# Performance work log

Measured on AMD Instinct MI355X. Metric: run time of the kernel, lower is better.

The kernel has to match this reference:

```python
import jax, jax.numpy as jnp
import numpy as np

V, E, D, L, B, EX = 50000, 128, 256, 400, 64, 200


def setup_inputs() -> dict:
    key = jax.random.key(0)
    ks = jax.random.split(key, 32)
    u = lambda k, shp, s=0.02: jax.random.uniform(k, shp, jnp.float32, -s, s)
    inp = {
        'input': jax.random.randint(ks[0], (B, 1), 0, V),
        'hidden_h': jax.random.normal(ks[1], (2, B, D), jnp.float32),
        'hidden_c': jax.random.normal(ks[2], (2, B, D), jnp.float32),
        'encoder_output': jax.random.normal(ks[3], (B, L, 2 * D), jnp.float32),
        'previous_context': jax.random.normal(ks[4], (B, 1, 2 * D), jnp.float32),
        'extended_input': jax.random.randint(ks[5], (B, L), 0, V + EX),
        'coverage': jax.random.uniform(ks[6], (B, L), jnp.float32),
        'padding_mask': jnp.ones((B, L), jnp.float32),
        'ex_size': EX,
        'output_step': 0,
        # parameters
        'emb_w': jax.random.normal(ks[7], (V, E), jnp.float32) * 1e-4,
        'lin_w': u(ks[8], (D, E + 2 * D)), 'lin_b': jnp.zeros((D,), jnp.float32),
        'w_ih': u(ks[9], (4 * D, D)), 'w_hh': u(ks[10], (4 * D, D)),
        'b_ih': jnp.zeros((4 * D,), jnp.float32).at[D:2 * D].set(1.0),
        'b_hh': jnp.zeros((4 * D,), jnp.float32),
        'red_h_w': u(ks[11], (D, 2 * D)), 'red_h_b': jnp.zeros((D,), jnp.float32),
        'red_c_w': u(ks[12], (D, 2 * D)), 'red_c_b': jnp.zeros((D,), jnp.float32),
        'wq_w': u(ks[13], (D, 2 * D)), 'wq_b': jnp.zeros((D,), jnp.float32),
        'cov_w': u(ks[14], (2 * D, 1)), 'cov_b': jnp.zeros((2 * D,), jnp.float32),
        'wk_w': u(ks[15], (D, 2 * D)), 'wk_b': jnp.zeros((D,), jnp.float32),
        'pre_w': u(ks[16], (D, 3 * D)), 'pre_b': jnp.zeros((D,), jnp.float32),
        'gen_w': u(ks[17], (V, D)), 'gen_b': jnp.zeros((V,), jnp.float32),
        'pgen_w': u(ks[18], (1, 5 * D)), 'pgen_b': jnp.zeros((1,), jnp.float32),
    }
    return inp


def reference(input, hidden_h, hidden_c, encoder_output, previous_context,
              extended_input, coverage, padding_mask, ex_size, output_step,
              emb_w, lin_w, lin_b, w_ih, w_hh, b_ih, b_hh,
              red_h_w, red_h_b, red_c_w, red_c_b,
              wq_w, wq_b, cov_w, cov_b, wk_w, wk_b,
              pre_w, pre_b, gen_w, gen_b, pgen_w, pgen_b):
    b = encoder_output.shape[0]
    d = w_ih.shape[1]
    scale = jnp.sqrt(jnp.float32(d))

    emb = emb_w[input[:, 0]][:, None, :]                      # [B,1,E]
    combine = jnp.concatenate([emb, previous_context], 2)     # [B,1,E+2D]
    x = combine @ lin_w.T + lin_b                             # [B,1,D]

    if output_step == 0:  # reduce bidirectional encoder state [2,B,D] -> [1,B,D]
        hs = jnp.transpose(hidden_h, (1, 0, 2)).reshape(b, 2 * d)
        cs = jnp.transpose(hidden_c, (1, 0, 2)).reshape(b, 2 * d)
        h = jax.nn.relu(hs @ red_h_w.T + red_h_b)
        c = jax.nn.relu(cs @ red_c_w.T + red_c_b)
    else:
        h, c = hidden_h[0], hidden_c[0]

    # single LSTM step (PyTorch gate order i,f,g,o)
    gates = x[:, 0] @ w_ih.T + b_ih + h @ w_hh.T + b_hh       # [B,4D]
    i, f, g, o = jnp.split(gates, 4, axis=1)
    c_new = jax.nn.sigmoid(f) * c + jax.nn.sigmoid(i) * jnp.tanh(g)
    h_new = jax.nn.sigmoid(o) * jnp.tanh(c_new)
    lstm_out = h_new[:, None, :]                              # [B,1,D]

    # scaled-dot coverage attention
    query = jnp.concatenate([h_new, c_new], 1)                # [B,2D]
    Q = jnp.tanh(query @ wq_w.T + wq_b)                       # [B,D]
    word_feature = encoder_output + (coverage[..., None] @ cov_w.T + cov_b)
    K = jnp.tanh(word_feature @ wk_w.T + wk_b)                # [B,L,D]
    score = jnp.einsum('bd,bld->bl', Q / scale, K)
    score = jnp.where(padding_mask > 0, score, jnp.float32(-1e18))
    attention = jax.nn.softmax(score, axis=1)                 # [B,L]
    weighted_context = jnp.einsum('bl,bld->bd', attention, encoder_output)[:, None, :]

    p_gen = jax.nn.sigmoid(
        jnp.concatenate([x[:, 0], weighted_context[:, 0], h_new, c_new], 1)
        @ pgen_w.T + pgen_b)                                  # [B,1]

    owc = jnp.concatenate([weighted_context, lstm_out], 2)[:, 0]  # [B,3D]
    pregen = owc @ pre_w.T + pre_b                            # [B,D]
    vocab_dist = p_gen * jax.nn.softmax(pregen @ gen_w.T + gen_b, axis=1)
    att_dist = (1.0 - p_gen) * attention                      # [B,L]

    vocab_ext = jnp.concatenate(
        [vocab_dist, jnp.zeros((b, ex_size), vocab_dist.dtype)], 1)
    final_dist = vocab_ext.at[jnp.arange(b)[:, None], extended_input].add(att_dist)

    hidden = (h_new[None], c_new[None])
    return (final_dist, hidden, weighted_context, attention, coverage, p_gen)
```

## Files before the change

kernel.cpp:

```cpp
#include <hip/hip_runtime.h>
#include <math.h>

#define BB 64
#define DD 256
#define LL 400
#define VV 50000
#define EE 128
#define NB 782

typedef __attribute__((ext_vector_type(8))) short short8v;
typedef __attribute__((ext_vector_type(4))) short short4v;
typedef __attribute__((ext_vector_type(4))) float f32x4;

__device__ __forceinline__ float sigmoidf_(float x){ return 1.0f/(1.0f+expf(-x)); }

__device__ __forceinline__ short f2bf(float f){
    unsigned u = __builtin_bit_cast(unsigned, f);
    u += 0x7fffu + ((u>>16)&1u);
    return (short)(u>>16);
}
__device__ __forceinline__ float bf2f(unsigned short b){
    unsigned u = ((unsigned)b) << 16;
    return __builtin_bit_cast(float, u);
}

#define ROW_X   0
#define ROW_WC  256
#define ROW_H   768
#define ROW_C   1024

#define DOT8(col, wptr, kk, acc) { \
    float a0_=(col)[((kk)+0)*64], a1_=(col)[((kk)+1)*64], a2_=(col)[((kk)+2)*64], a3_=(col)[((kk)+3)*64], \
          a4_=(col)[((kk)+4)*64], a5_=(col)[((kk)+5)*64], a6_=(col)[((kk)+6)*64], a7_=(col)[((kk)+7)*64]; \
    asm volatile("" : "+v"(a0_),"+v"(a1_),"+v"(a2_),"+v"(a3_),"+v"(a4_),"+v"(a5_),"+v"(a6_),"+v"(a7_)); \
    acc += a0_*(wptr)[(kk)+0] + a1_*(wptr)[(kk)+1] + a2_*(wptr)[(kk)+2] + a3_*(wptr)[(kk)+3] \
         + a4_*(wptr)[(kk)+4] + a5_*(wptr)[(kk)+5] + a6_*(wptr)[(kk)+6] + a7_*(wptr)[(kk)+7]; }

__device__ __forceinline__ float dot4v(f32x4 a, f32x4 b){
    return a[0]*b[0] + a[1]*b[1] + a[2]*b[2] + a[3]*b[3];
}

__global__ __launch_bounds__(256) void k_front1(
    const int* __restrict__ inp, const float* __restrict__ hh, const float* __restrict__ hc,
    const float* __restrict__ prev, const float* __restrict__ emb_w,
    const float* __restrict__ lin_w, const float* __restrict__ lin_b,
    const float* __restrict__ rhw, const float* __restrict__ rhb,
    const float* __restrict__ rcw, const float* __restrict__ rcb,
    const int* __restrict__ step_p,
    const float* __restrict__ wk_w, const float* __restrict__ wk_b,
    const float* __restrict__ cov_w, const float* __restrict__ cov_b,
    float* __restrict__ actT, float* __restrict__ WhT, float* __restrict__ WcT0,
    short* __restrict__ Wb, float* __restrict__ u, float* __restrict__ v2,
    float* __restrict__ wcpart, float* __restrict__ Ssum)
{
    const int d = blockIdx.x, y = blockIdx.y, t = threadIdx.x;
    const int b = t >> 2, kq = t & 3;
    __shared__ float lw[640];
    __shared__ float red[256];

    if (y == 3){
        if (t < 128) wcpart[d*128 + t] = 0.f;
        if (d == 0 && t >= 128 && t < 192) Ssum[t-128] = 0.f;
        const float* row = wk_w + (size_t)d*512;
        float su=0.f, sv=0.f;
        for (int j=t; j<512; j+=256){
            float wv = row[j];
            Wb[(size_t)(j>>3)*2048 + d*8 + (j&7)] = f2bf(wv);
            su += wv*cov_w[j];
            sv += wv*cov_b[j];
        }
        float* rs = lw;
        float* rv = red;
        rs[t]=su; rv[t]=sv; __syncthreads();
        for (int s=128;s>0;s>>=1){ if(t<s){rs[t]+=rs[t+s]; rv[t]+=rv[t+s];} __syncthreads(); }
        if (t==0){ u[d]=rs[0]; v2[d]=rv[0] + wk_b[d]; }
        return;
    }

    if (y == 0){
        if (t < 160) ((f32x4*)lw)[t] = ((const f32x4*)(lin_w + (size_t)d*640))[t];
        __syncthreads();
        const f32x4* lw4 = (const f32x4*)lw;
        const f32x4* er4 = (const f32x4*)(emb_w + (size_t)inp[b]*EE);
        const f32x4* pv4 = (const f32x4*)(prev + (size_t)b*512);
        float acc = 0.f;
        for (int i=kq; i<160; i+=16){
            f32x4 v0 = (i    < 32) ? er4[i]    : pv4[i-32];
            f32x4 v1 = (i+4  < 32) ? er4[i+4]  : pv4[i-28];
            f32x4 v2_ = pv4[i-24];
            f32x4 v3 = pv4[i-20];
            if (i+8  < 32) v2_ = er4[i+8];
            if (i+12 < 32) v3 = er4[i+12];
            asm volatile("" : "+v"(v0),"+v"(v1),"+v"(v2_),"+v"(v3));
            acc += dot4v(v0, lw4[i]) + dot4v(v1, lw4[i+4])
                 + dot4v(v2_, lw4[i+8]) + dot4v(v3, lw4[i+12]);
        }
        acc += __shfl_xor(acc,1); acc += __shfl_xor(acc,2);
        if (kq == 0) actT[(ROW_X + d)*64 + b] = lin_b[d] + acc;
        return;
    }

    const float* src  = (y==1) ? hh  : hc;
    float*       dstT = (y==1) ? WhT : WcT0;
    if (*step_p == 0){
        const float* wrow = ((y==1) ? rhw : rcw) + (size_t)d*512;
        const float  bias = ((y==1) ? rhb : rcb)[d];
        if (t < 128) ((f32x4*)lw)[t] = ((const f32x4*)wrow)[t];
        __syncthreads();
        const f32x4* lw4 = (const f32x4*)lw;
        const f32x4* s0 = (const f32x4*)(src + (size_t)b*DD);
        const f32x4* s1 = (const f32x4*)(src + (size_t)BB*DD + (size_t)b*DD);
        float acc = 0.f;
        for (int i=kq; i<128; i+=16){
            f32x4 v0 = (i    < 64) ? s0[i]    : s1[i-64];
            f32x4 v1 = (i+4  < 64) ? s0[i+4]  : s1[i-60];
            f32x4 v2_ = (i+8 < 64) ? s0[i+8]  : s1[i-56];
            f32x4 v3 = (i+12 < 64) ? s0[i+12] : s1[i-52];
            asm volatile("" : "+v"(v0),"+v"(v1),"+v"(v2_),"+v"(v3));
            acc += dot4v(v0, lw4[i]) + dot4v(v1, lw4[i+4])
                 + dot4v(v2_, lw4[i+8]) + dot4v(v3, lw4[i+12]);
        }
        acc += __shfl_xor(acc,1); acc += __shfl_xor(acc,2);
        if (kq == 0){
            float a = bias + acc;
            dstT[d*64 + b] = a>0.f ? a : 0.f;
        }
    } else {
        if (t < 64) dstT[d*64 + t] = src[(size_t)t*DD + d];
    }
}

__global__ __launch_bounds__(256) void k_gl(
    const float* __restrict__ actT, const float* __restrict__ WhT, const float* __restrict__ WcT0,
    const float* __restrict__ w_ih, const float* __restrict__ w_hh,
    const float* __restrict__ b_ih, const float* __restrict__ b_hh,
    float* __restrict__ o_h, float* __restrict__ o_c, float* __restrict__ actT_out)
{
    const int d = blockIdx.x, t = threadIdx.x;
    const int b = t & 63, gi = t >> 6;
    __shared__ float wih[4][256];
    __shared__ float whh[4][256];
    __shared__ float gl[4][64];

    const int gr = gi*DD + d;
    ((f32x4*)&wih[gi][0])[b] = ((const f32x4*)(w_ih + (size_t)gr*DD))[b];
    ((f32x4*)&whh[gi][0])[b] = ((const f32x4*)(w_hh + (size_t)gr*DD))[b];
    __syncthreads();

    const float* xcol = actT + ROW_X*64 + b;
    const float* hcol = WhT + b;
    float a0=0.f, a1=0.f;
    for (int kk=0; kk<256; kk+=8){
        DOT8(xcol, &wih[gi][0], kk, a0);
        DOT8(hcol, &whh[gi][0], kk, a1);
    }
    gl[gi][b] = a0 + a1 + b_ih[gr] + b_hh[gr];
    __syncthreads();

    if (t < 64){
        float iv = sigmoidf_(gl[0][t]);
        float fv = sigmoidf_(gl[1][t]);
        float gv = tanhf(gl[2][t]);
        float ov = sigmoidf_(gl[3][t]);
        float cn = fv*WcT0[d*64 + t] + iv*gv;
        float hn = ov*tanhf(cn);
        o_c[(size_t)t*DD + d] = cn;
        o_h[(size_t)t*DD + d] = hn;
        actT_out[(ROW_C + d)*64 + t] = cn;
        actT_out[(ROW_H + d)*64 + t] = hn;
    }
}

__global__ __launch_bounds__(256) void k_q2(
    const float* __restrict__ actT,
    const float* __restrict__ wq_w, const float* __restrict__ wq_b,
    float* __restrict__ Qs)
{
    const int d = blockIdx.x, t = threadIdx.x;
    const int b = t & 63, w = t >> 6;
    __shared__ float lw[512];
    __shared__ float red[4][64];
    if (t < 128) ((f32x4*)lw)[t] = ((const f32x4*)(wq_w + (size_t)d*512))[t];
    __syncthreads();
    const float* col = actT + ROW_H*64 + b;
    float acc = 0.f;
    const int k0 = w*128;
    for (int kk=k0; kk<k0+128; kk+=8)
        DOT8(col, lw, kk, acc);
    red[w][b] = acc; __syncthreads();
    if (t < 64)
        Qs[(size_t)t*DD + d] = tanhf(wq_b[d] + red[0][t]+red[1][t]+red[2][t]+red[3][t]) * 0.0625f;
}

#define SC_MFMA(KS, BF) \
  { const int cc_ = (KS)*4 + qw; \
    short8v a0_ = *(const short8v*)&As[lr*512 + ((cc_ ^ (lr&7))<<3)]; \
    short8v a1_ = *(const short8v*)&As[(16+lr)*512 + ((cc_ ^ (lr&7))<<3)]; \
    acc0 = __builtin_amdgcn_mfma_f32_16x16x32_bf16(a0_, BF, acc0, 0,0,0); \
    acc1 = __builtin_amdgcn_mfma_f32_16x16x32_bf16(a1_, BF, acc1, 0,0,0); }

#define SC_CHUNK(KC, B0,B1,B2,B3) \
    SC_MFMA((KC)*4+0, B0); SC_MFMA((KC)*4+1, B1); \
    SC_MFMA((KC)*4+2, B2); SC_MFMA((KC)*4+3, B3);

__global__ __launch_bounds__(1024, 4) void k_score_mfma(
    const float* __restrict__ enc, const short* __restrict__ Wb,
    const float* __restrict__ u, const float* __restrict__ v2,
    const float* __restrict__ Qs, const float* __restrict__ cov,
    const float* __restrict__ pmask,
    float* __restrict__ Ev, float* __restrict__ Ssum, float* __restrict__ wcpart)
{
    const int b  = blockIdx.y;
    const int l0 = blockIdx.x * 32;
    const int tid = threadIdx.x;
    const int wave = tid >> 6, lane = tid & 63;
    const int qw = lane >> 4, lr = lane & 15;
    const int col = wave*16 + lr;

    __shared__ __align__(16) short As[32*512];
    __shared__ float Red[16][32];
    __shared__ float esh[32];

    const short* bp = Wb + (size_t)qw*2048 + col*8;
    short8v c0 = *(const short8v*)(bp +  0*8192);
    short8v c1 = *(const short8v*)(bp +  1*8192);
    short8v c2 = *(const short8v*)(bp +  2*8192);
    short8v c3 = *(const short8v*)(bp +  3*8192);

    const int arow = tid >> 5;
    const int af   = tid & 31;
    const bool aval = (l0 + arow) < LL;
    const float4* aptr = (const float4*)(enc + ((size_t)(b*LL + (aval ? l0+arow : 0)))*512);
    float4 areg[4];
    #pragma unroll
    for (int j=0; j<4; j++)
        areg[j] = aval ? aptr[af + j*32] : float4{0.f,0.f,0.f,0.f};

    #pragma unroll
    for (int j=0; j<4; j++){
        const int fi   = af + j*32;
        const int c    = fi >> 1;
        const int half = fi & 1;
        const int cs   = c ^ (arow & 7);
        short4v t4;
        t4[0]=f2bf(areg[j].x); t4[1]=f2bf(areg[j].y);
        t4[2]=f2bf(areg[j].z); t4[3]=f2bf(areg[j].w);
        *(short4v*)&As[arow*512 + cs*8 + half*4] = t4;
    }
    __syncthreads();

    f32x4 acc0 = f32x4{0.f,0.f,0.f,0.f};
    f32x4 acc1 = f32x4{0.f,0.f,0.f,0.f};

    short8v n0 = *(const short8v*)(bp +  4*8192);
    short8v n1 = *(const short8v*)(bp +  5*8192);
    short8v n2 = *(const short8v*)(bp +  6*8192);
    short8v n3 = *(const short8v*)(bp +  7*8192);
    SC_CHUNK(0, c0,c1,c2,c3);
    asm volatile("" : "+v"(n0),"+v"(n1),"+v"(n2),"+v"(n3));

    c0 = *(const short8v*)(bp +  8*8192);
    c1 = *(const short8v*)(bp +  9*8192);
    c2 = *(const short8v*)(bp + 10*8192);
    c3 = *(const short8v*)(bp + 11*8192);
    SC_CHUNK(1, n0,n1,n2,n3);
    asm volatile("" : "+v"(c0),"+v"(c1),"+v"(c2),"+v"(c3));

    n0 = *(const short8v*)(bp + 12*8192);
    n1 = *(const short8v*)(bp + 13*8192);
    n2 = *(const short8v*)(bp + 14*8192);
    n3 = *(const short8v*)(bp + 15*8192);
    SC_CHUNK(2, c0,c1,c2,c3);
    asm volatile("" : "+v"(n0),"+v"(n1),"+v"(n2),"+v"(n3));

    SC_CHUNK(3, n0,n1,n2,n3);

    const float qv = Qs[b*DD + col];
    const float uv = u[col];
    const float vv = v2[col];
    #pragma unroll
    for (int rf=0; rf<2; rf++){
        const f32x4 acc = rf ? acc1 : acc0;
        const int rbase = l0 + rf*16 + qw*4;
        float cv[4];
        if (rbase < LL){
            float4 c4v = *(const float4*)(cov + (size_t)b*LL + rbase);
            cv[0]=c4v.x; cv[1]=c4v.y; cv[2]=c4v.z; cv[3]=c4v.w;
        } else { cv[0]=cv[1]=cv[2]=cv[3]=0.f; }
        #pragma unroll
        for (int r=0; r<4; r++){
            float s = qv * tanhf(acc[r] + cv[r]*uv + vv);
            s += __shfl_xor(s,1); s += __shfl_xor(s,2);
            s += __shfl_xor(s,4); s += __shfl_xor(s,8);
            if (lr == 0) Red[wave][rf*16 + qw*4 + r] = s;
        }
    }
    __syncthreads();
    if (tid < 32){
        int l = l0 + tid;
        float e = 0.f;
        if (l < LL){
            float s = 0.f;
            #pragma unroll
            for (int w2=0; w2<16; w2++) s += Red[w2][tid];
            e = (pmask[b*LL+l] > 0.f) ? expf(s) : 0.f;
            Ev[b*LL + l] = e;
        }
        esh[tid] = e;
        float se = e;
        se += __shfl_xor(se,1); se += __shfl_xor(se,2);
        se += __shfl_xor(se,4); se += __shfl_xor(se,8);
        se += __shfl_xor(se,16);
        if (tid == 0) atomicAdd(&Ssum[b], se);
    }
    __syncthreads();
    if (tid < 512){
        const int c  = tid >> 3;
        const int p  = tid & 7;
        float acc = 0.f;
        #pragma unroll
        for (int l=0; l<32; l++){
            unsigned short bits = (unsigned short)As[l*512 + ((c ^ (l&7))<<3) + p];
            acc += esh[l] * bf2f(bits);
        }
        atomicAdd(&wcpart[b*512 + tid], acc);
    }
}

__global__ __launch_bounds__(512) void k_attn(
    const float* __restrict__ Ev, const float* __restrict__ Ssum,
    const float* __restrict__ cov_in,
    float* __restrict__ attn_out, float* __restrict__ cov_out)
{
    const int b = blockIdx.x, t = threadIdx.x;
    if (t < LL){
        const float inv = 1.0f / Ssum[b];
        attn_out[b*LL + t] = Ev[b*LL + t] * inv;
        cov_out[b*LL + t]  = cov_in[b*LL + t];
    }
}

__global__ __launch_bounds__(256) void k_tr(const float* __restrict__ wcpart,
                                            const float* __restrict__ Ssum,
                                            float* __restrict__ o_wc,
                                            float* __restrict__ actT)
{
    const int j0 = blockIdx.x * 64;
    __shared__ float tile[64][65];
    __shared__ float invs[64];
    const int t = threadIdx.x;
    const int c = t & 63, r0 = t >> 6;
    if (t < 64) invs[t] = 1.0f / Ssum[t];
    __syncthreads();
    #pragma unroll
    for (int bb = r0; bb < 64; bb += 4){
        float v = wcpart[(size_t)bb*512 + j0 + c] * invs[bb];
        tile[bb][c] = v;
        o_wc[(size_t)bb*512 + j0 + c] = v;
    }
    __syncthreads();
    #pragma unroll
    for (int jj = r0; jj < 64; jj += 4)
        actT[(ROW_WC + j0 + jj)*64 + c] = tile[c][jj];
}

__global__ __launch_bounds__(256) void k_pregen(
    const float* __restrict__ actT,
    const float* __restrict__ pre_w, const float* __restrict__ pre_b,
    const float* __restrict__ pgen_w, const float* __restrict__ pgen_b,
    short* __restrict__ pregenb, float* __restrict__ pgen_out)
{
    const int d = blockIdx.x, t = threadIdx.x;
    const int b = t & 63, w = t >> 6;
    __shared__ float pw[768];
    __shared__ float red[4][64];
    if (t < 192) ((f32x4*)pw)[t] = ((const f32x4*)(pre_w + (size_t)d*768))[t];
    __syncthreads();
    const float* col = actT + ROW_WC*64 + b;
    float acc = 0.f;
    const int k0 = w*192;
    for (int kk=k0; kk<k0+192; kk+=8)
        DOT8(col, pw, kk, acc);
    red[w][b] = acc; __syncthreads();
    if (t < 64)
        pregenb[(size_t)t*DD + d] = f2bf(pre_b[d] + red[0][t]+red[1][t]+red[2][t]+red[3][t]);

    if (blockIdx.x == 0){
        __syncthreads();
        const float* colx = actT + b;
        float p = 0.f;
        const int j0 = w*320;
        for (int jj=j0; jj<j0+320; jj+=8)
            DOT8(colx, pgen_w, jj, p);
        red[w][b] = p; __syncthreads();
        if (t < 64)
            pgen_out[t] = sigmoidf_(red[0][t]+red[1][t]+red[2][t]+red[3][t] + pgen_b[0]);
    }
}

#define GEN_SLICE(KS, RA, RB) \
  { short8v bb_; \
    bb_[0]=f2bf(RA[0]); bb_[1]=f2bf(RA[1]); bb_[2]=f2bf(RA[2]); bb_[3]=f2bf(RA[3]); \
    bb_[4]=f2bf(RB[0]); bb_[5]=f2bf(RB[1]); bb_[6]=f2bf(RB[2]); bb_[7]=f2bf(RB[3]); \
    const int cc_ = (KS)*4 + qw; \
    const int cs_ = (cc_ ^ (lr&7))<<3; \
    short8v aa0_ = *(const short8v*)&As[(lr     )*256 + cs_]; \
    short8v aa1_ = *(const short8v*)&As[(16+lr)*256 + cs_]; \
    short8v aa2_ = *(const short8v*)&As[(32+lr)*256 + cs_]; \
    short8v aa3_ = *(const short8v*)&As[(48+lr)*256 + cs_]; \
    acc0 = __builtin_amdgcn_mfma_f32_16x16x32_bf16(aa0_, bb_, acc0, 0,0,0); \
    acc1 = __builtin_amdgcn_mfma_f32_16x16x32_bf16(aa1_, bb_, acc1, 0,0,0); \
    acc2 = __builtin_amdgcn_mfma_f32_16x16x32_bf16(aa2_, bb_, acc2, 0,0,0); \
    acc3 = __builtin_amdgcn_mfma_f32_16x16x32_bf16(aa3_, bb_, acc3, 0,0,0); }

__global__ __launch_bounds__(256, 3) void k_gen_mfma(
    const short* __restrict__ pregenb, const float* __restrict__ gen_w,
    const float* __restrict__ gen_b, short* __restrict__ lgb,
    float* __restrict__ blkM, float* __restrict__ blkS)
{
    const int blk = blockIdx.x;
    const int v0 = blk * 64;
    const int tid = threadIdx.x;
    const int wave = tid>>6, lane = tid&63, qw = lane>>4, lr = lane&15;

    __shared__ __align__(16) short As[64*256];
    __shared__ float pm[4][64];
    __shared__ float ps[4][64];

    const int vrow = v0 + wave*16 + lr;
    const bool bval = (vrow < VV);
    const f32x4* bq = (const f32x4*)(gen_w + (size_t)(bval ? vrow : 0)*DD + qw*8);
    f32x4 a0 = bq[ 0], a1 = bq[ 1];
    f32x4 a2 = bq[ 8], a3 = bq[ 9];
    f32x4 a4 = bq[16], a5 = bq[17];
    f32x4 a6 = bq[24], a7 = bq[25];

    #pragma unroll
    for (int j=0; j<8; j++){
        int f = tid + j*256;
        int row = f >> 5, c = f & 31;
        short8v s = ((const short8v*)pregenb)[f];
        *(short8v*)&As[row*256 + ((c ^ (row&7))<<3)] = s;
    }
    __syncthreads();

    f32x4 acc0 = f32x4{0.f,0.f,0.f,0.f};
    f32x4 acc1 = f32x4{0.f,0.f,0.f,0.f};
    f32x4 acc2 = f32x4{0.f,0.f,0.f,0.f};
    f32x4 acc3 = f32x4{0.f,0.f,0.f,0.f};

    f32x4 b0 = bq[32], b1 = bq[33];
    f32x4 b2 = bq[40], b3 = bq[41];
    f32x4 b4 = bq[48], b5 = bq[49];
    f32x4 b6 = bq[56], b7 = bq[57];

    GEN_SLICE(0, a0, a1);
    GEN_SLICE(1, a2, a3);
    GEN_SLICE(2, a4, a5);
    GEN_SLICE(3, a6, a7);
    asm volatile("" : "+v"(b0),"+v"(b1),"+v"(b2),"+v"(b3),
                      "+v"(b4),"+v"(b5),"+v"(b6),"+v"(b7));
    GEN_SLICE(4, b0, b1);
    GEN_SLICE(5, b2, b3);
    GEN_SLICE(6, b4, b5);
    GEN_SLICE(7, b6, b7);

    f32x4 accs[4] = {acc0, acc1, acc2, acc3};
    const int v = v0 + wave*16 + lr;
    const bool vv = (v < VV);
    const float gb = vv ? gen_b[v] : 0.f;
    #pragma unroll
    for (int rf=0; rf<4; rf++){
        #pragma unroll
        for (int r=0; r<4; r++){
            float lg = accs[rf][r] + gb;
            int bt = rf*16 + qw*4 + r;
            if (vv) lgb[(size_t)bt*VV + v] = f2bf(lg);
            float x = vv ? lg : -1e30f;
            float mx = x;
            mx = fmaxf(mx, __shfl_xor(mx,1));
            mx = fmaxf(mx, __shfl_xor(mx,2));
            mx = fmaxf(mx, __shfl_xor(mx,4));
            mx = fmaxf(mx, __shfl_xor(mx,8));
            float e = vv ? expf(x - mx) : 0.f;
            e += __shfl_xor(e,1); e += __shfl_xor(e,2);
            e += __shfl_xor(e,4); e += __shfl_xor(e,8);
            if (lr == 0){ pm[wave][bt] = mx; ps[wave][bt] = e; }
        }
    }
    __syncthreads();
    if (tid < 64){
        float M = fmaxf(fmaxf(pm[0][tid], pm[1][tid]), fmaxf(pm[2][tid], pm[3][tid]));
        float S = ps[0][tid]*expf(pm[0][tid]-M) + ps[1][tid]*expf(pm[1][tid]-M)
                + ps[2][tid]*expf(pm[2][tid]-M) + ps[3][tid]*expf(pm[3][tid]-M);
        blkM[(size_t)tid*NB + blk] = M;
        blkS[(size_t)tid*NB + blk] = S;
    }
}

__global__ __launch_bounds__(256) void k_vred(
    const float* __restrict__ blkM, const float* __restrict__ blkS,
    float* __restrict__ Ms, float* __restrict__ Ss)
{
    const int b = blockIdx.x, t = threadIdx.x;
    __shared__ float red[256];
    float m = -INFINITY;
    for (int i=t; i<NB; i+=256) m = fmaxf(m, blkM[(size_t)b*NB + i]);
    red[t]=m; __syncthreads();
    for (int s=128;s>0;s>>=1){ if(t<s) red[t]=fmaxf(red[t],red[t+s]); __syncthreads(); }
    const float M = red[0]; __syncthreads();
    float s = 0.f;
    for (int i=t; i<NB; i+=256) s += blkS[(size_t)b*NB + i] * expf(blkM[(size_t)b*NB + i] - M);
    red[t]=s; __syncthreads();
    for (int st=128;st>0;st>>=1){ if(t<st) red[t]+=red[t+st]; __syncthreads(); }
    if (t==0){ Ms[b]=M; Ss[b]=red[0]; }
}

__global__ void k_final(const short* __restrict__ lgb, float* __restrict__ out,
                        const float* __restrict__ Ms, const float* __restrict__ Ss,
                        const float* __restrict__ pgen, int W)
{
    size_t idx = (size_t)blockIdx.x*blockDim.x + threadIdx.x;
    if (idx >= (size_t)BB*W) return;
    int b = (int)(idx / W);
    int v = (int)(idx % W);
    float* row = out + (size_t)b*W;
    if (v < VV){
        float lg = bf2f((unsigned short)lgb[(size_t)b*VV + v]);
        row[v] = pgen[b] * expf(lg - Ms[b]) / Ss[b];
    } else row[v] = 0.f;
}

__global__ void k_scatter(float* __restrict__ out, const int* __restrict__ ext,
                          const float* __restrict__ attn, const float* __restrict__ pgen, int W)
{
    int idx = blockIdx.x*blockDim.x + threadIdx.x;
    if (idx >= BB*LL) return;
    int b = idx / LL;
    atomicAdd(out + (size_t)b*W + ext[idx], (1.0f - pgen[b]) * attn[idx]);
}

extern "C" void kernel_launch(void* const* d_in, const int* in_sizes, int n_in,
                              void* d_out, int out_size, void* d_ws, size_t ws_size,
                              hipStream_t stream)
{
    const int*   inp     = (const int*)  d_in[0];
    const float* hh      = (const float*)d_in[1];
    const float* hc      = (const float*)d_in[2];
    const float* enc     = (const float*)d_in[3];
    const float* prev    = (const float*)d_in[4];
    const int*   ext     = (const int*)  d_in[5];
    const float* cov     = (const float*)d_in[6];
    const float* pmask   = (const float*)d_in[7];
    const int*   step_p  = (const int*)  d_in[9];
    const float* emb_w   = (const float*)d_in[10];
    const float* lin_w   = (const float*)d_in[11];
    const float* lin_b   = (const float*)d_in[12];
    const float* w_ih    = (const float*)d_in[13];
    const float* w_hh    = (const float*)d_in[14];
    const float* b_ih    = (const float*)d_in[15];
    const float* b_hh    = (const float*)d_in[16];
    const float* rhw     = (const float*)d_in[17];
    const float* rhb     = (const float*)d_in[18];
    const float* rcw     = (const float*)d_in[19];
    const float* rcb     = (const float*)d_in[20];
    const float* wq_w    = (const float*)d_in[21];
    const float* wq_b    = (const float*)d_in[22];
    const float* cov_w   = (const float*)d_in[23];
    const float* cov_b   = (const float*)d_in[24];
    const float* wk_w    = (const float*)d_in[25];
    const float* wk_b    = (const float*)d_in[26];
    const float* pre_w   = (const float*)d_in[27];
    const float* pre_b   = (const float*)d_in[28];
    const float* gen_w   = (const float*)d_in[29];
    const float* gen_b   = (const float*)d_in[30];
    const float* pgen_w  = (const float*)d_in[31];
    const float* pgen_b  = (const float*)d_in[32];

    const int W = out_size / BB - 4*DD - 2*LL - 1;
    float* out     = (float*)d_out;
    float* o_final = out;
    float* o_h     = out + (size_t)BB*W;
    float* o_c     = o_h + BB*DD;
    float* o_wc    = o_c + BB*DD;
    float* o_attn  = o_wc + BB*2*DD;
    float* o_cov   = o_attn + BB*LL;
    float* o_pgen  = o_cov + BB*LL;

    float* W_actT   = (float*)d_ws;
    float* W_whT    = W_actT + 1280*64;
    float* W_wcT0   = W_whT + BB*DD;
    float* W_q      = W_wcT0 + BB*DD;
    float* W_e      = W_q + BB*DD;
    float* W_S      = W_e + BB*LL;
    float* W_wcp    = W_S + BB;
    float* W_m      = W_wcp + BB*512;
    float* W_s      = W_m + BB;
    float* W_u      = W_s + BB;
    float* W_v2     = W_u + DD;
    float* W_blkM   = W_v2 + DD;
    float* W_blkS   = W_blkM + (size_t)BB*NB;
    short* W_wb     = (short*)(W_blkS + (size_t)BB*NB);
    short* W_pgb    = (short*)(W_wb + 64*2048);
    short* W_lg     = W_pgb + BB*DD;

    k_front1<<<dim3(DD,4), 256, 0, stream>>>(inp, hh, hc, prev, emb_w, lin_w, lin_b,
                                             rhw, rhb, rcw, rcb, step_p,
                                             wk_w, wk_b, cov_w, cov_b,
                                             W_actT, W_whT, W_wcT0, W_wb, W_u, W_v2,
                                             W_wcp, W_S);
    k_gl<<<DD, 256, 0, stream>>>(W_actT, W_whT, W_wcT0, w_ih, w_hh, b_ih, b_hh,
                                 o_h, o_c, W_actT);
    k_q2<<<DD, 256, 0, stream>>>(W_actT, wq_w, wq_b, W_q);
    k_score_mfma<<<dim3(13, BB), 1024, 0, stream>>>(enc, W_wb, W_u, W_v2, W_q, cov, pmask,
                                                    W_e, W_S, W_wcp);
    k_attn<<<BB, 512, 0, stream>>>(W_e, W_S, cov, o_attn, o_cov);
    k_tr<<<8, 256, 0, stream>>>(W_wcp, W_S, o_wc, W_actT);
    k_pregen<<<DD, 256, 0, stream>>>(W_actT, pre_w, pre_b, pgen_w, pgen_b, W_pgb, o_pgen);
    k_gen_mfma<<<NB, 256, 0, stream>>>(W_pgb, gen_w, gen_b, W_lg, W_blkM, W_blkS);
    k_vred<<<BB, 256, 0, stream>>>(W_blkM, W_blkS, W_m, W_s);
    k_final<<<(int)(((size_t)BB*W+255)/256), 256, 0, stream>>>(W_lg, o_final, W_m, W_s, o_pgen, W);
    k_scatter<<<(BB*LL+255)/256, 256, 0, stream>>>(o_final, ext, o_attn, o_pgen, W);
}
```

Before: 132.4 us.

## Stage score-kernel weight tiles through double-buffered LDS instead of per-wave registers

The score MFMA kernel now loads each weight chunk cooperatively, with each thread fetching contiguous 16-byte pieces, and stores it into a double-buffered shared-memory tile. Waves then read their B fragments from LDS, replacing the earlier scattered direct global loads into registers with manual prefetch. The launch-bounds occupancy hint is also dropped. This adds 64KB of LDS per block and a __syncthreads per chunk, which cuts occupancy and adds sync overhead in exchange for coalesced weight loads.

```diff
diff --git a/kernel.cpp b/kernel.cpp
--- a/kernel.cpp
+++ b/kernel.cpp
@@ -192,18 +192,7 @@
         Qs[(size_t)t*DD + d] = tanhf(wq_b[d] + red[0][t]+red[1][t]+red[2][t]+red[3][t]) * 0.0625f;
 }
 
-#define SC_MFMA(KS, BF) \
-  { const int cc_ = (KS)*4 + qw; \
-    short8v a0_ = *(const short8v*)&As[lr*512 + ((cc_ ^ (lr&7))<<3)]; \
-    short8v a1_ = *(const short8v*)&As[(16+lr)*512 + ((cc_ ^ (lr&7))<<3)]; \
-    acc0 = __builtin_amdgcn_mfma_f32_16x16x32_bf16(a0_, BF, acc0, 0,0,0); \
-    acc1 = __builtin_amdgcn_mfma_f32_16x16x32_bf16(a1_, BF, acc1, 0,0,0); }
-
-#define SC_CHUNK(KC, B0,B1,B2,B3) \
-    SC_MFMA((KC)*4+0, B0); SC_MFMA((KC)*4+1, B1); \
-    SC_MFMA((KC)*4+2, B2); SC_MFMA((KC)*4+3, B3);
-
-__global__ __launch_bounds__(1024, 4) void k_score_mfma(
+__global__ __launch_bounds__(1024) void k_score_mfma(
     const float* __restrict__ enc, const short* __restrict__ Wb,
     const float* __restrict__ u, const float* __restrict__ v2,
     const float* __restrict__ Qs, const float* __restrict__ cov,
@@ -218,14 +207,9 @@
     const int col = wave*16 + lr;
 
     __shared__ __align__(16) short As[32*512];
+    __shared__ __align__(16) short Bs[2][16384];
     __shared__ float Red[16][32];
     __shared__ float esh[32];
-
-    const short* bp = Wb + (size_t)qw*2048 + col*8;
-    short8v c0 = *(const short8v*)(bp +  0*8192);
-    short8v c1 = *(const short8v*)(bp +  1*8192);
-    short8v c2 = *(const short8v*)(bp +  2*8192);
-    short8v c3 = *(const short8v*)(bp +  3*8192);
 
     const int arow = tid >> 5;
     const int af   = tid & 31;
@@ -235,7 +219,6 @@
     #pragma unroll
     for (int j=0; j<4; j++)
         areg[j] = aval ? aptr[af + j*32] : float4{0.f,0.f,0.f,0.f};
-
     #pragma unroll
     for (int j=0; j<4; j++){
         const int fi   = af + j*32;
@@ -247,33 +230,41 @@
         t4[2]=f2bf(areg[j].z); t4[3]=f2bf(areg[j].w);
         *(short4v*)&As[arow*512 + cs*8 + half*4] = t4;
     }
-    __syncthreads();
+
+    const short* wp = Wb + (size_t)tid*8;
+    short8v t0 = *(const short8v*)(wp);
+    short8v t1 = *(const short8v*)(wp + 8192);
 
     f32x4 acc0 = f32x4{0.f,0.f,0.f,0.f};
     f32x4 acc1 = f32x4{0.f,0.f,0.f,0.f};
 
-    short8v n0 = *(const short8v*)(bp +  4*8192);
-    short8v n1 = *(const short8v*)(bp +  5*8192);
-    short8v n2 = *(const short8v*)(bp +  6*8192);
-    short8v n3 = *(const short8v*)(bp +  7*8192);
-    SC_CHUNK(0, c0,c1,c2,c3);
-    asm volatile("" : "+v"(n0),"+v"(n1),"+v"(n2),"+v"(n3));
-
-    c0 = *(const short8v*)(bp +  8*8192);
-    c1 = *(const short8v*)(bp +  9*8192);
-    c2 = *(const short8v*)(bp + 10*8192);
-    c3 = *(const short8v*)(bp + 11*8192);
-    SC_CHUNK(1, n0,n1,n2,n3);
-    asm volatile("" : "+v"(c0),"+v"(c1),"+v"(c2),"+v"(c3));
-
-    n0 = *(const short8v*)(bp + 12*8192);
-    n1 = *(const short8v*)(bp + 13*8192);
-    n2 = *(const short8v*)(bp + 14*8192);
-    n3 = *(const short8v*)(bp + 15*8192);
-    SC_CHUNK(2, c0,c1,c2,c3);
-    asm volatile("" : "+v"(n0),"+v"(n1),"+v"(n2),"+v"(n3));
-
-    SC_CHUNK(3, n0,n1,n2,n3);
+    #pragma unroll
+    for (int c=0; c<8; ++c){
+        const int cur = c & 1;
+        *(short8v*)&Bs[cur][tid*8]        = t0;
+        *(short8v*)&Bs[cur][tid*8 + 8192] = t1;
+        if (c < 7){
+            t0 = *(const short8v*)(wp + (c+1)*16384);
+            t1 = *(const short8v*)(wp + (c+1)*16384 + 8192);
+        }
+        __syncthreads();
+        #pragma unroll
+        for (int ks2=0; ks2<2; ks2++){
+            const int kgl = ks2*4 + qw;
+            short8v bf = *(const short8v*)&Bs[cur][kgl*2048 + col*8];
+            const int cc = (c*2 + ks2)*4 + qw;
+            {
+                const int r = lr;
+                short8v a = *(const short8v*)&As[r*512 + ((cc ^ (r&7))<<3)];
+                acc0 = __builtin_amdgcn_mfma_f32_16x16x32_bf16(a, bf, acc0, 0,0,0);
+            }
+            {
+                const int r = 16 + lr;
+                short8v a = *(const short8v*)&As[r*512 + ((cc ^ (r&7))<<3)];
+                acc1 = __builtin_amdgcn_mfma_f32_16x16x32_bf16(a, bf, acc1, 0,0,0);
+            }
+        }
+    }
 
     const float qv = Qs[b*DD + col];
     const float uv = u[col];
```

After: 146.2 us. +10.5%, slower.
